# Optimization experiments

Measured on AMD Instinct MI355X. Metric: run time of the kernel, lower is better.

Reference implementation:

```python
import jax, jax.numpy as jnp
import numpy as np

T, B, N_INP, N_HID, N_OUT = 512, 128, 256, 1024, 128


def setup_inputs() -> dict:
    key = jax.random.key(0)
    ks = jax.random.split(key, 7)
    x = jax.random.normal(ks[0], (T, B, N_INP), dtype=jnp.float32)
    # PyTorch RNNCell/Linear default init: U(-1/sqrt(fan_in), 1/sqrt(fan_in))
    s_h = 1.0 / np.sqrt(N_HID)
    W_ih = jax.random.uniform(ks[1], (N_HID, N_INP), jnp.float32, -s_h, s_h)
    W_hh = jax.random.uniform(ks[2], (N_HID, N_HID), jnp.float32, -s_h, s_h)
    b_ih = jax.random.uniform(ks[3], (N_HID,), jnp.float32, -s_h, s_h)
    b_hh = jax.random.uniform(ks[4], (N_HID,), jnp.float32, -s_h, s_h)
    W_ro = jax.random.uniform(ks[5], (N_OUT, N_HID), jnp.float32, -s_h, s_h)
    b_ro = jax.random.uniform(ks[6], (N_OUT,), jnp.float32, -s_h, s_h)
    return {"x": x, "W_ih": W_ih, "W_hh": W_hh, "b_ih": b_ih,
            "b_hh": b_hh, "W_ro": W_ro, "b_ro": b_ro}


def reference(x, W_ih, W_hh, b_ih, b_hh, W_ro, b_ro):
    # x: [T, B, n_inp]; recurrence: state = tanh(x_t W_ih^T + b_ih + state W_hh^T + b_hh)
    batch = x.shape[1]
    n_hid = W_hh.shape[0]
    state0 = jnp.zeros((batch, n_hid), dtype=x.dtype)

    # Precompute the input projection for all timesteps in one big GEMM.
    x_proj = jnp.einsum('tbi,hi->tbh', x, W_ih) + b_ih + b_hh  # [T, B, n_hid]

    def step(state, xp_t):
        new_state = jnp.tanh(xp_t + state @ W_hh.T)
        return new_state, None

    final_state, _ = jax.lax.scan(step, state0, x_proj)
    # readout applied to final hidden state only (stateOnly=None path)
    return final_state @ W_ro.T + b_ro  # [B, n_out]
```

## Files before the change

kernel.cpp:

```cpp
#include <hip/hip_runtime.h>
#include <hip/hip_bf16.h>
#include <stdint.h>


#define TSTEPS 512
#define BATCH  128
#define NI     256
#define NH     1024
#define NO     128
#define NBLK   128
#define NTHR   512
#define NWAVE  8
#define BG     16
#define COLS   64

typedef __attribute__((ext_vector_type(8))) short s16x8;
typedef __attribute__((ext_vector_type(4))) float f32x4;
typedef __attribute__((ext_vector_type(4))) unsigned u32x4;
typedef unsigned long long ull;

__device__ __forceinline__ unsigned short f2bf_rne(float f) {
  unsigned u = __builtin_bit_cast(unsigned, f);
  unsigned r = u + 0x7fffu + ((u >> 16) & 1u);
  return (unsigned short)(r >> 16);
}
__device__ __forceinline__ float bf2f(unsigned short h) {
  unsigned u = ((unsigned)h) << 16;
  return __builtin_bit_cast(float, u);
}
__device__ __forceinline__ void split_bf(float v, short &hi, short &lo) {
  unsigned short h = f2bf_rne(v);
  hi = (short)h;
  lo = (short)f2bf_rne(v - bf2f(h));
}
__device__ __forceinline__ f32x4 mfma16(s16x8 a, s16x8 b, f32x4 c) {
  return __builtin_amdgcn_mfma_f32_16x16x32_bf16(a, b, c, 0, 0, 0);
}
__device__ __forceinline__ float fast_tanh(float a) {
  float cl = fminf(fmaxf(a, -15.f), 15.f);
  float e  = __expf(2.f * cl);
  return (e - 1.f) / (e + 1.f);
}

#define SIDX(g, w, r, k) ((((size_t)(g) * NWAVE + (w)) * BG + (r)) * 128 + (k))

__global__ __launch_bounds__(NTHR, 2)
void rnn_persistent(const float* __restrict__ x,
                    const float* __restrict__ W_ih,
                    const float* __restrict__ W_hh,
                    const float* __restrict__ b_ih,
                    const float* __restrict__ b_hh,
                    unsigned*    __restrict__ SP)
{
  const int tid  = threadIdx.x;
  const int wave = tid >> 6;
  const int lane = tid & 63;
  const int lr   = lane & 15;
  const int lq   = lane >> 4;
  const int g    = blockIdx.x >> 4;
  const int m    = blockIdx.x & 15;
  const int row0 = g * BG;
  const int h0   = m * COLS;
  const int kq0  = wave * 128;
  const int iq0  = wave * 32;

  __shared__ float red[2][NWAVE][1024];

  s16x8 whh_hi[4][4], whh_lo[4][4];
  #pragma unroll
  for (int nt = 0; nt < 4; ++nt) {
    const int h = h0 + nt * 16 + lr;
    #pragma unroll
    for (int kb = 0; kb < 4; ++kb) {
      const float* p = W_hh + (size_t)h * NH + kq0 + kb * 32 + lq * 8;
      s16x8 hi, lo;
      #pragma unroll
      for (int j = 0; j < 8; ++j) { short a, b; split_bf(p[j], a, b); hi[j] = a; lo[j] = b; }
      whh_hi[nt][kb] = hi; whh_lo[nt][kb] = lo;
    }
  }
  s16x8 wih_hi[4], wih_lo[4];
  #pragma unroll
  for (int nt = 0; nt < 4; ++nt) {
    const int h = h0 + nt * 16 + lr;
    const float* p = W_ih + (size_t)h * NI + iq0 + lq * 8;
    s16x8 hi, lo;
    #pragma unroll
    for (int j = 0; j < 8; ++j) { short a, b; split_bf(p[j], a, b); hi[j] = a; lo[j] = b; }
    wih_hi[nt] = hi; wih_lo[nt] = lo;
  }

  const int er = tid >> 5;
  const int ec = (tid & 31) * 2;
  const float bias0 = b_ih[h0 + ec]     + b_hh[h0 + ec];
  const float bias1 = b_ih[h0 + ec + 1] + b_hh[h0 + ec + 1];
  const int wsl = m >> 1;
  const int klo = (m & 1) * 64 + ec;

  unsigned* buf0 = SP;
  unsigned* buf1 = SP + (size_t)BATCH * NH;

  float xf[8];
  {
    const float* xp = x + (size_t)(row0 + lr) * NI + iq0 + lq * 8;
    #pragma unroll
    for (int j = 0; j < 8; ++j) xf[j] = xp[j];
  }

  const unsigned* sb0 = buf0 + SIDX(g, wave, lr, lq * 8);
  const unsigned* sb1 = buf1 + SIDX(g, wave, lr, lq * 8);

  for (int t = 0; t < TSTEPS; ++t) {
    f32x4 acc[4];
    #pragma unroll
    for (int nt = 0; nt < 4; ++nt) acc[nt] = (f32x4){0.f, 0.f, 0.f, 0.f};
    {
      s16x8 xhi, xlo;
      #pragma unroll
      for (int j = 0; j < 8; ++j) { short a, b; split_bf(xf[j], a, b); xhi[j] = a; xlo[j] = b; }
      #pragma unroll
      for (int nt = 0; nt < 4; ++nt) {
        acc[nt] = mfma16(xhi, wih_hi[nt], acc[nt]);
        acc[nt] = mfma16(xhi, wih_lo[nt], acc[nt]);
        acc[nt] = mfma16(xlo, wih_hi[nt], acc[nt]);
      }
    }
    const unsigned etag = (unsigned)((t >> 1) & 1);
    const unsigned* sb = (t & 1) ? sb1 : sb0;
    u32x4 sv0, sv1, sv2, sv3, sv4, sv5, sv6, sv7;
    {
      const u32x4 e4 = (u32x4){etag, etag, etag, etag};
      for (;;) {
        asm volatile(
          "global_load_dwordx4 %0, %8, off sc1\n\t"
          "global_load_dwordx4 %1, %8, off offset:16 sc1\n\t"
          "global_load_dwordx4 %2, %8, off offset:128 sc1\n\t"
          "global_load_dwordx4 %3, %8, off offset:144 sc1\n\t"
          "global_load_dwordx4 %4, %8, off offset:256 sc1\n\t"
          "global_load_dwordx4 %5, %8, off offset:272 sc1\n\t"
          "global_load_dwordx4 %6, %8, off offset:384 sc1\n\t"
          "global_load_dwordx4 %7, %8, off offset:400 sc1\n\t"
          "s_waitcnt vmcnt(0)"
          : "=&v"(sv0), "=&v"(sv1), "=&v"(sv2), "=&v"(sv3),
            "=&v"(sv4), "=&v"(sv5), "=&v"(sv6), "=&v"(sv7)
          : "v"(sb) : "memory");
        u32x4 b4 = (sv0 ^ e4) | (sv1 ^ e4) | (sv2 ^ e4) | (sv3 ^ e4)
                 | (sv4 ^ e4) | (sv5 ^ e4) | (sv6 ^ e4) | (sv7 ^ e4);
        unsigned bad = b4[0] | b4[1] | b4[2] | b4[3];
        if ((bad & 1u) == 0) break;
      }
    }
    {
      const int tn = (t + 1 < TSTEPS) ? (t + 1) : t;
      const float* xp = x + (size_t)tn * BATCH * NI + (size_t)(row0 + lr) * NI + iq0 + lq * 8;
      #pragma unroll
      for (int j = 0; j < 8; ++j) xf[j] = xp[j];
    }
    {
      unsigned sw[32];
      #pragma unroll
      for (int e = 0; e < 4; ++e) {
        sw[0  + e] = sv0[e]; sw[4  + e] = sv1[e];
        sw[8  + e] = sv2[e]; sw[12 + e] = sv3[e];
        sw[16 + e] = sv4[e]; sw[20 + e] = sv5[e];
        sw[24 + e] = sv6[e]; sw[28 + e] = sv7[e];
      }
      #pragma unroll
      for (int kb = 0; kb < 4; ++kb) {
        s16x8 shi, slo;
        #pragma unroll
        for (int j = 0; j < 8; ++j) {
          unsigned w = sw[kb * 8 + j];
          shi[j] = (short)(w >> 16);
          slo[j] = (short)(w & 0xffffu);
        }
        #pragma unroll
        for (int nt = 0; nt < 4; ++nt) {
          acc[nt] = mfma16(shi, whh_hi[nt][kb], acc[nt]);
          acc[nt] = mfma16(shi, whh_lo[nt][kb], acc[nt]);
          acc[nt] = mfma16(slo, whh_hi[nt][kb], acc[nt]);
        }
      }
    }
    const int rbi = t & 1;
    #pragma unroll
    for (int nt = 0; nt < 4; ++nt)
      #pragma unroll
      for (int r = 0; r < 4; ++r)
        red[rbi][wave][(lq * 4 + r) * 64 + nt * 16 + lr] = acc[nt][r];
    __syncthreads();
    {
      float s0 = bias0, s1 = bias1;
      #pragma unroll
      for (int w = 0; w < NWAVE; ++w) {
        float2 v = *(const float2*)&red[rbi][w][er * 64 + ec];
        s0 += v.x; s1 += v.y;
      }
      float t0 = fast_tanh(s0), t1 = fast_tanh(s1);
      const unsigned otag = (unsigned)(((t + 1) >> 1) & 1);
      unsigned short h0b = f2bf_rne(t0);
      unsigned       l0b = ((f2bf_rne(t0 - bf2f(h0b)) & 0xfffeu) | otag);
      unsigned short h1b = f2bf_rne(t1);
      unsigned       l1b = ((f2bf_rne(t1 - bf2f(h1b)) & 0xfffeu) | otag);
      ull pk = ((ull)(((unsigned)h1b << 16) | l1b) << 32)
             |  (ull)(((unsigned)h0b << 16) | l0b);
      ull* op = (ull*)(((t + 1) & 1 ? buf1 : buf0) + SIDX(g, wsl, er, klo));
      __hip_atomic_store(op, pk, __ATOMIC_RELAXED, __HIP_MEMORY_SCOPE_AGENT);
    }
  }
}

__global__ __launch_bounds__(256)
void init_buf1(unsigned* __restrict__ SP) {
  const int i = blockIdx.x * 256 + threadIdx.x;
  SP[BATCH * NH + i] = 1u;
}

__global__ __launch_bounds__(512)
void rnn_readout(const unsigned* __restrict__ SP,
                 const float* __restrict__ W_ro,
                 const float* __restrict__ b_ro,
                 float* __restrict__ out)
{
  __shared__ float srow[4][NH];
  const int b0 = blockIdx.x * 4;
  for (int i = threadIdx.x; i < 4 * NH; i += 512) {
    const int b = b0 + (i >> 10);
    const int h = i & 1023;
    unsigned u = SP[SIDX(b >> 4, h >> 7, b & 15, h & 127)];
    srow[i >> 10][h] = bf2f((unsigned short)(u >> 16)) + bf2f((unsigned short)(u & 0xffffu));
  }
  __syncthreads();
  const int bb = threadIdx.x >> 7;
  const int o  = threadIdx.x & 127;
  const float* wr = W_ro + (size_t)o * NH;
  float s = 0.f;
  #pragma unroll 4
  for (int k = 0; k < NH; ++k) s += srow[bb][k] * wr[k];
  out[(size_t)(b0 + bb) * NO + o] = s + b_ro[o];
}

extern "C" void kernel_launch(void* const* d_in, const int* in_sizes, int n_in,
                              void* d_out, int out_size, void* d_ws, size_t ws_size,
                              hipStream_t stream) {
  (void)in_sizes; (void)n_in; (void)out_size; (void)ws_size;
  const float* x    = (const float*)d_in[0];
  const float* W_ih = (const float*)d_in[1];
  const float* W_hh = (const float*)d_in[2];
  const float* b_ih = (const float*)d_in[3];
  const float* b_hh = (const float*)d_in[4];
  const float* W_ro = (const float*)d_in[5];
  const float* b_ro = (const float*)d_in[6];
  float* out = (float*)d_out;

  unsigned* SP = (unsigned*)d_ws;

  hipMemsetAsync(SP, 0, (size_t)BATCH * NH * sizeof(unsigned), stream);
  init_buf1<<<(BATCH * NH) / 256, 256, 0, stream>>>(SP);

  rnn_persistent<<<NBLK, NTHR, 0, stream>>>(x, W_ih, W_hh, b_ih, b_hh, SP);
  rnn_readout<<<BATCH / 4, 512, 0, stream>>>(SP, W_ro, b_ro, out);
}
```

Before: 1.944 ms.

## Drop low-order weight split and widen blocks to 128 hidden columns

Weights are now held only as a single bf16 term instead of a hi/lo split, so each state chunk needs two MFMAs per tile instead of three. The grid shrinks from 128 to 64 persistent blocks, each covering 128 hidden columns. That halves the number of blocks taking part in the per-step cross-block flag synchronisation and makes the freed register space usable for the wider tile. The shared reduction buffer becomes single-buffered and gets an extra barrier, and each thread packs and stores four outputs. Precision drops because the weights lose their low-order residual, which may raise error over 512 recurrent steps.

```diff
diff --git a/kernel.cpp b/kernel.cpp
--- a/kernel.cpp
+++ b/kernel.cpp
@@ -8,11 +8,11 @@
 #define NI     256
 #define NH     1024
 #define NO     128
-#define NBLK   128
+#define NBLK   64
 #define NTHR   512
 #define NWAVE  8
 #define BG     16
-#define COLS   64
+#define COLS   128
 
 typedef __attribute__((ext_vector_type(8))) short s16x8;
 typedef __attribute__((ext_vector_type(4))) float f32x4;
@@ -42,7 +42,7 @@
   return (e - 1.f) / (e + 1.f);
 }
 
-#define SIDX(g, w, r, k) ((((size_t)(g) * NWAVE + (w)) * BG + (r)) * 128 + (k))
+#define SIDX(g, p, r, k) ((((size_t)(g) * NWAVE + (p)) * BG + (r)) * 128 + (k))
 
 __global__ __launch_bounds__(NTHR, 2)
 void rnn_persistent(const float* __restrict__ x,
@@ -57,45 +57,44 @@
   const int lane = tid & 63;
   const int lr   = lane & 15;
   const int lq   = lane >> 4;
-  const int g    = blockIdx.x >> 4;
-  const int m    = blockIdx.x & 15;
+  const int g    = blockIdx.x & 7;
+  const int p    = blockIdx.x >> 3;
   const int row0 = g * BG;
-  const int h0   = m * COLS;
+  const int h0   = p * COLS;
   const int kq0  = wave * 128;
   const int iq0  = wave * 32;
 
-  __shared__ float red[2][NWAVE][1024];
-
-  s16x8 whh_hi[4][4], whh_lo[4][4];
+  __shared__ float red[NWAVE][BG][COLS];
+
+  s16x8 whh[8][4];
   #pragma unroll
-  for (int nt = 0; nt < 4; ++nt) {
+  for (int nt = 0; nt < 8; ++nt) {
     const int h = h0 + nt * 16 + lr;
     #pragma unroll
     for (int kb = 0; kb < 4; ++kb) {
-      const float* p = W_hh + (size_t)h * NH + kq0 + kb * 32 + lq * 8;
-      s16x8 hi, lo;
-      #pragma unroll
-      for (int j = 0; j < 8; ++j) { short a, b; split_bf(p[j], a, b); hi[j] = a; lo[j] = b; }
-      whh_hi[nt][kb] = hi; whh_lo[nt][kb] = lo;
-    }
-  }
-  s16x8 wih_hi[4], wih_lo[4];
+      const float* pw = W_hh + (size_t)h * NH + kq0 + kb * 32 + lq * 8;
+      s16x8 hi;
+      #pragma unroll
+      for (int j = 0; j < 8; ++j) hi[j] = (short)f2bf_rne(pw[j]);
+      whh[nt][kb] = hi;
+    }
+  }
+  s16x8 wih[8];
   #pragma unroll
-  for (int nt = 0; nt < 4; ++nt) {
+  for (int nt = 0; nt < 8; ++nt) {
     const int h = h0 + nt * 16 + lr;
-    const float* p = W_ih + (size_t)h * NI + iq0 + lq * 8;
-    s16x8 hi, lo;
-    #pragma unroll
-    for (int j = 0; j < 8; ++j) { short a, b; split_bf(p[j], a, b); hi[j] = a; lo[j] = b; }
-    wih_hi[nt] = hi; wih_lo[nt] = lo;
+    const float* pw = W_ih + (size_t)h * NI + iq0 + lq * 8;
+    s16x8 hi;
+    #pragma unroll
+    for (int j = 0; j < 8; ++j) hi[j] = (short)f2bf_rne(pw[j]);
+    wih[nt] = hi;
   }
 
   const int er = tid >> 5;
-  const int ec = (tid & 31) * 2;
-  const float bias0 = b_ih[h0 + ec]     + b_hh[h0 + ec];
-  const float bias1 = b_ih[h0 + ec + 1] + b_hh[h0 + ec + 1];
-  const int wsl = m >> 1;
-  const int klo = (m & 1) * 64 + ec;
+  const int ec = (tid & 31) * 4;
+  float bias[4];
+  #pragma unroll
+  for (int j = 0; j < 4; ++j) bias[j] = b_ih[h0 + ec + j] + b_hh[h0 + ec + j];
 
   unsigned* buf0 = SP;
   unsigned* buf1 = SP + (size_t)BATCH * NH;
@@ -111,18 +110,17 @@
   const unsigned* sb1 = buf1 + SIDX(g, wave, lr, lq * 8);
 
   for (int t = 0; t < TSTEPS; ++t) {
-    f32x4 acc[4];
-    #pragma unroll
-    for (int nt = 0; nt < 4; ++nt) acc[nt] = (f32x4){0.f, 0.f, 0.f, 0.f};
+    f32x4 acc[8];
+    #pragma unroll
+    for (int nt = 0; nt < 8; ++nt) acc[nt] = (f32x4){0.f, 0.f, 0.f, 0.f};
     {
       s16x8 xhi, xlo;
       #pragma unroll
       for (int j = 0; j < 8; ++j) { short a, b; split_bf(xf[j], a, b); xhi[j] = a; xlo[j] = b; }
       #pragma unroll
-      for (int nt = 0; nt < 4; ++nt) {
-        acc[nt] = mfma16(xhi, wih_hi[nt], acc[nt]);
-        acc[nt] = mfma16(xhi, wih_lo[nt], acc[nt]);
-        acc[nt] = mfma16(xlo, wih_hi[nt], acc[nt]);
+      for (int nt = 0; nt < 8; ++nt) {
+        acc[nt] = mfma16(xhi, wih[nt], acc[nt]);
+        acc[nt] = mfma16(xlo, wih[nt], acc[nt]);
       }
     }
     const unsigned etag = (unsigned)((t >> 1) & 1);
@@ -156,56 +154,51 @@
       #pragma unroll
       for (int j = 0; j < 8; ++j) xf[j] = xp[j];
     }
-    {
-      unsigned sw[32];
-      #pragma unroll
-      for (int e = 0; e < 4; ++e) {
-        sw[0  + e] = sv0[e]; sw[4  + e] = sv1[e];
-        sw[8  + e] = sv2[e]; sw[12 + e] = sv3[e];
-        sw[16 + e] = sv4[e]; sw[20 + e] = sv5[e];
-        sw[24 + e] = sv6[e]; sw[28 + e] = sv7[e];
-      }
-      #pragma unroll
-      for (int kb = 0; kb < 4; ++kb) {
-        s16x8 shi, slo;
-        #pragma unroll
-        for (int j = 0; j < 8; ++j) {
-          unsigned w = sw[kb * 8 + j];
-          shi[j] = (short)(w >> 16);
-          slo[j] = (short)(w & 0xffffu);
-        }
-        #pragma unroll
-        for (int nt = 0; nt < 4; ++nt) {
-          acc[nt] = mfma16(shi, whh_hi[nt][kb], acc[nt]);
-          acc[nt] = mfma16(shi, whh_lo[nt][kb], acc[nt]);
-          acc[nt] = mfma16(slo, whh_hi[nt][kb], acc[nt]);
-        }
-      }
-    }
-    const int rbi = t & 1;
-    #pragma unroll
-    for (int nt = 0; nt < 4; ++nt)
+    #pragma unroll
+    for (int kb = 0; kb < 4; ++kb) {
+      const u32x4 va = (kb == 0) ? sv0 : (kb == 1) ? sv2 : (kb == 2) ? sv4 : sv6;
+      const u32x4 vb = (kb == 0) ? sv1 : (kb == 1) ? sv3 : (kb == 2) ? sv5 : sv7;
+      s16x8 shi, slo;
+      #pragma unroll
+      for (int i = 0; i < 4; ++i) {
+        unsigned wa = va[i], wb = vb[i];
+        shi[i]     = (short)(wa >> 16); slo[i]     = (short)(wa & 0xffffu);
+        shi[i + 4] = (short)(wb >> 16); slo[i + 4] = (short)(wb & 0xffffu);
+      }
+      #pragma unroll
+      for (int nt = 0; nt < 8; ++nt) {
+        acc[nt] = mfma16(shi, whh[nt][kb], acc[nt]);
+        acc[nt] = mfma16(slo, whh[nt][kb], acc[nt]);
+      }
+    }
+    __syncthreads();
+    #pragma unroll
+    for (int nt = 0; nt < 8; ++nt)
       #pragma unroll
       for (int r = 0; r < 4; ++r)
-        red[rbi][wave][(lq * 4 + r) * 64 + nt * 16 + lr] = acc[nt][r];
+        red[wave][lq * 4 + r][nt * 16 + lr] = acc[nt][r];
     __syncthreads();
     {
-      float s0 = bias0, s1 = bias1;
+      float s[4] = {bias[0], bias[1], bias[2], bias[3]};
       #pragma unroll
       for (int w = 0; w < NWAVE; ++w) {
-        float2 v = *(const float2*)&red[rbi][w][er * 64 + ec];
-        s0 += v.x; s1 += v.y;
-      }
-      float t0 = fast_tanh(s0), t1 = fast_tanh(s1);
+        const f32x4 v = *(const f32x4*)&red[w][er][ec];
+        s[0] += v[0]; s[1] += v[1]; s[2] += v[2]; s[3] += v[3];
+      }
       const unsigned otag = (unsigned)(((t + 1) >> 1) & 1);
-      unsigned short h0b = f2bf_rne(t0);
-      unsigned       l0b = ((f2bf_rne(t0 - bf2f(h0b)) & 0xfffeu) | otag);
-      unsigned short h1b = f2bf_rne(t1);
-      unsigned       l1b = ((f2bf_rne(t1 - bf2f(h1b)) & 0xfffeu) | otag);
-      ull pk = ((ull)(((unsigned)h1b << 16) | l1b) << 32)
-             |  (ull)(((unsigned)h0b << 16) | l0b);
-      ull* op = (ull*)(((t + 1) & 1 ? buf1 : buf0) + SIDX(g, wsl, er, klo));
-      __hip_atomic_store(op, pk, __ATOMIC_RELAXED, __HIP_MEMORY_SCOPE_AGENT);
+      unsigned pkw[4];
+      #pragma unroll
+      for (int j = 0; j < 4; ++j) {
+        float tv = fast_tanh(s[j]);
+        unsigned short hb = f2bf_rne(tv);
+        unsigned       lb = ((f2bf_rne(tv - bf2f(hb)) & 0xfffeu) | otag);
+        pkw[j] = (((unsigned)hb) << 16) | lb;
+      }
+      ull pk01 = ((ull)pkw[1] << 32) | (ull)pkw[0];
+      ull pk23 = ((ull)pkw[3] << 32) | (ull)pkw[2];
+      ull* op = (ull*)(((t + 1) & 1 ? buf1 : buf0) + SIDX(g, p, er, ec));
+      __hip_atomic_store(op,     pk01, __ATOMIC_RELAXED, __HIP_MEMORY_SCOPE_AGENT);
+      __hip_atomic_store(op + 1, pk23, __ATOMIC_RELAXED, __HIP_MEMORY_SCOPE_AGENT);
     }
   }
 }
```

New measurement: 2.177 ms. 12.0% more time.

## Pack hi/lo bf16 pairs per dword and duplicate weights to cut MFMA count

Applied to the files above, without the earlier changes.

Replaces the three-MFMA hi/lo split-bf16 product with a packed form. Each state and input dword keeps its hi/lo bf16 halves together, and every weight is rounded once to bf16 and duplicated, so one MFMA over the K dimension forms (hi+lo)*w. This cuts recurrent MFMAs per step and removes the unpacking shuffles, but it drops the weight low-order correction, which lowers accuracy. The state loads are now issued before the input-projection MFMAs to overlap the polling latency, and the block-to-(group,column) mapping is swapped.

```diff
diff --git a/kernel.cpp b/kernel.cpp
--- a/kernel.cpp
+++ b/kernel.cpp
@@ -28,11 +28,6 @@
   unsigned u = ((unsigned)h) << 16;
   return __builtin_bit_cast(float, u);
 }
-__device__ __forceinline__ void split_bf(float v, short &hi, short &lo) {
-  unsigned short h = f2bf_rne(v);
-  hi = (short)h;
-  lo = (short)f2bf_rne(v - bf2f(h));
-}
 __device__ __forceinline__ f32x4 mfma16(s16x8 a, s16x8 b, f32x4 c) {
   return __builtin_amdgcn_mfma_f32_16x16x32_bf16(a, b, c, 0, 0, 0);
 }
@@ -41,8 +36,38 @@
   float e  = __expf(2.f * cl);
   return (e - 1.f) / (e + 1.f);
 }
+__device__ __forceinline__ unsigned packf(float v) {
+  unsigned short h = f2bf_rne(v);
+  unsigned short l = f2bf_rne(v - bf2f(h));
+  return (((unsigned)h) << 16) | (unsigned)l;
+}
 
 #define SIDX(g, w, r, k) ((((size_t)(g) * NWAVE + (w)) * BG + (r)) * 128 + (k))
+
+#define SWEEP_ISSUE(PTR)                                                   \
+  asm volatile(                                                            \
+    "global_load_dwordx4 %0, %8, off sc1\n\t"                              \
+    "global_load_dwordx4 %1, %8, off offset:64 sc1\n\t"                    \
+    "global_load_dwordx4 %2, %8, off offset:128 sc1\n\t"                   \
+    "global_load_dwordx4 %3, %8, off offset:192 sc1\n\t"                   \
+    "global_load_dwordx4 %4, %8, off offset:256 sc1\n\t"                   \
+    "global_load_dwordx4 %5, %8, off offset:320 sc1\n\t"                   \
+    "global_load_dwordx4 %6, %8, off offset:384 sc1\n\t"                   \
+    "global_load_dwordx4 %7, %8, off offset:448 sc1"                       \
+    : "=&v"(sv0), "=&v"(sv1), "=&v"(sv2), "=&v"(sv3),                      \
+      "=&v"(sv4), "=&v"(sv5), "=&v"(sv6), "=&v"(sv7)                       \
+    : "v"(PTR) : "memory")
+
+#define SWEEP_WAIT()                                                       \
+  asm volatile("s_waitcnt vmcnt(0)"                                        \
+    : "+v"(sv0), "+v"(sv1), "+v"(sv2), "+v"(sv3),                          \
+      "+v"(sv4), "+v"(sv5), "+v"(sv6), "+v"(sv7) :: "memory");             \
+  __builtin_amdgcn_sched_barrier(0)
+
+#define TAGCHECK(OUT)                                                      \
+  { u32x4 b4 = (sv0 ^ e4) | (sv1 ^ e4) | (sv2 ^ e4) | (sv3 ^ e4)           \
+             | (sv4 ^ e4) | (sv5 ^ e4) | (sv6 ^ e4) | (sv7 ^ e4);          \
+    OUT = (b4[0] | b4[1] | b4[2] | b4[3]) & 1u; }
 
 __global__ __launch_bounds__(NTHR, 2)
 void rnn_persistent(const float* __restrict__ x,
@@ -57,8 +82,8 @@
   const int lane = tid & 63;
   const int lr   = lane & 15;
   const int lq   = lane >> 4;
-  const int g    = blockIdx.x >> 4;
-  const int m    = blockIdx.x & 15;
+  const int g    = blockIdx.x & 7;
+  const int m    = blockIdx.x >> 3;
   const int row0 = g * BG;
   const int h0   = m * COLS;
   const int kq0  = wave * 128;
@@ -66,28 +91,33 @@
 
   __shared__ float red[2][NWAVE][1024];
 
-  s16x8 whh_hi[4][4], whh_lo[4][4];
+  s16x8 whhd[4][4][2];
   #pragma unroll
   for (int nt = 0; nt < 4; ++nt) {
     const int h = h0 + nt * 16 + lr;
     #pragma unroll
-    for (int kb = 0; kb < 4; ++kb) {
-      const float* p = W_hh + (size_t)h * NH + kq0 + kb * 32 + lq * 8;
-      s16x8 hi, lo;
-      #pragma unroll
-      for (int j = 0; j < 8; ++j) { short a, b; split_bf(p[j], a, b); hi[j] = a; lo[j] = b; }
-      whh_hi[nt][kb] = hi; whh_lo[nt][kb] = lo;
-    }
-  }
-  s16x8 wih_hi[4], wih_lo[4];
+    for (int kb = 0; kb < 4; ++kb)
+      #pragma unroll
+      for (int p = 0; p < 2; ++p) {
+        const float* pw = W_hh + (size_t)h * NH + kq0 + kb * 32 + p * 16 + lq * 4;
+        s16x8 f;
+        #pragma unroll
+        for (int j = 0; j < 8; ++j) f[j] = (short)f2bf_rne(pw[j >> 1]);
+        whhd[nt][kb][p] = f;
+      }
+  }
+  s16x8 wihd[4][2];
   #pragma unroll
   for (int nt = 0; nt < 4; ++nt) {
     const int h = h0 + nt * 16 + lr;
-    const float* p = W_ih + (size_t)h * NI + iq0 + lq * 8;
-    s16x8 hi, lo;
-    #pragma unroll
-    for (int j = 0; j < 8; ++j) { short a, b; split_bf(p[j], a, b); hi[j] = a; lo[j] = b; }
-    wih_hi[nt] = hi; wih_lo[nt] = lo;
+    #pragma unroll
+    for (int p = 0; p < 2; ++p) {
+      const float* pw = W_ih + (size_t)h * NI + iq0 + p * 16 + lq * 4;
+      s16x8 f;
+      #pragma unroll
+      for (int j = 0; j < 8; ++j) f[j] = (short)f2bf_rne(pw[j >> 1]);
+      wihd[nt][p] = f;
+    }
   }
 
   const int er = tid >> 5;
@@ -100,87 +130,79 @@
   unsigned* buf0 = SP;
   unsigned* buf1 = SP + (size_t)BATCH * NH;
 
-  float xf[8];
+  s16x8 xfA, xfB;
   {
-    const float* xp = x + (size_t)(row0 + lr) * NI + iq0 + lq * 8;
-    #pragma unroll
-    for (int j = 0; j < 8; ++j) xf[j] = xp[j];
-  }
-
-  const unsigned* sb0 = buf0 + SIDX(g, wave, lr, lq * 8);
-  const unsigned* sb1 = buf1 + SIDX(g, wave, lr, lq * 8);
+    const float* xp = x + (size_t)(row0 + lr) * NI + iq0 + lq * 4;
+    f32x4 v0 = *(const f32x4*)xp;
+    f32x4 v1 = *(const f32x4*)(xp + 16);
+    u32x4 a, b;
+    #pragma unroll
+    for (int d = 0; d < 4; ++d) { a[d] = packf(v0[d]); b[d] = packf(v1[d]); }
+    xfA = __builtin_bit_cast(s16x8, a);
+    xfB = __builtin_bit_cast(s16x8, b);
+  }
+
+  const unsigned* sb0 = buf0 + SIDX(g, wave, lr, lq * 4);
+  const unsigned* sb1 = buf1 + SIDX(g, wave, lr, lq * 4);
 
   for (int t = 0; t < TSTEPS; ++t) {
-    f32x4 acc[4];
-    #pragma unroll
-    for (int nt = 0; nt < 4; ++nt) acc[nt] = (f32x4){0.f, 0.f, 0.f, 0.f};
-    {
-      s16x8 xhi, xlo;
-      #pragma unroll
-      for (int j = 0; j < 8; ++j) { short a, b; split_bf(xf[j], a, b); xhi[j] = a; xlo[j] = b; }
-      #pragma unroll
-      for (int nt = 0; nt < 4; ++nt) {
-        acc[nt] = mfma16(xhi, wih_hi[nt], acc[nt]);
-        acc[nt] = mfma16(xhi, wih_lo[nt], acc[nt]);
-        acc[nt] = mfma16(xlo, wih_hi[nt], acc[nt]);
-      }
-    }
     const unsigned etag = (unsigned)((t >> 1) & 1);
     const unsigned* sb = (t & 1) ? sb1 : sb0;
     u32x4 sv0, sv1, sv2, sv3, sv4, sv5, sv6, sv7;
+    SWEEP_ISSUE(sb);
+    f32x4 acc[4];
+    #pragma unroll
+    for (int nt = 0; nt < 4; ++nt) acc[nt] = (f32x4){0.f, 0.f, 0.f, 0.f};
+    #pragma unroll
+    for (int nt = 0; nt < 4; ++nt) {
+      acc[nt] = mfma16(xfA, wihd[nt][0], acc[nt]);
+      acc[nt] = mfma16(xfB, wihd[nt][1], acc[nt]);
+    }
     {
       const u32x4 e4 = (u32x4){etag, etag, etag, etag};
-      for (;;) {
-        asm volatile(
-          "global_load_dwordx4 %0, %8, off sc1\n\t"
-          "global_load_dwordx4 %1, %8, off offset:16 sc1\n\t"
-          "global_load_dwordx4 %2, %8, off offset:128 sc1\n\t"
-          "global_load_dwordx4 %3, %8, off offset:144 sc1\n\t"
-          "global_load_dwordx4 %4, %8, off offset:256 sc1\n\t"
-          "global_load_dwordx4 %5, %8, off offset:272 sc1\n\t"
-          "global_load_dwordx4 %6, %8, off offset:384 sc1\n\t"
-          "global_load_dwordx4 %7, %8, off offset:400 sc1\n\t"
-          "s_waitcnt vmcnt(0)"
-          : "=&v"(sv0), "=&v"(sv1), "=&v"(sv2), "=&v"(sv3),
-            "=&v"(sv4), "=&v"(sv5), "=&v"(sv6), "=&v"(sv7)
-          : "v"(sb) : "memory");
-        u32x4 b4 = (sv0 ^ e4) | (sv1 ^ e4) | (sv2 ^ e4) | (sv3 ^ e4)
-                 | (sv4 ^ e4) | (sv5 ^ e4) | (sv6 ^ e4) | (sv7 ^ e4);
-        unsigned bad = b4[0] | b4[1] | b4[2] | b4[3];
-        if ((bad & 1u) == 0) break;
-      }
-    }
+      unsigned bad;
+      SWEEP_WAIT();
+      TAGCHECK(bad);
+      while (bad) {
+        SWEEP_ISSUE(sb);
+        SWEEP_WAIT();
+        TAGCHECK(bad);
+      }
+    }
+    f32x4 xv0, xv1;
     {
       const int tn = (t + 1 < TSTEPS) ? (t + 1) : t;
-      const float* xp = x + (size_t)tn * BATCH * NI + (size_t)(row0 + lr) * NI + iq0 + lq * 8;
-      #pragma unroll
-      for (int j = 0; j < 8; ++j) xf[j] = xp[j];
-    }
-    {
-      unsigned sw[32];
-      #pragma unroll
-      for (int e = 0; e < 4; ++e) {
-        sw[0  + e] = sv0[e]; sw[4  + e] = sv1[e];
-        sw[8  + e] = sv2[e]; sw[12 + e] = sv3[e];
-        sw[16 + e] = sv4[e]; sw[20 + e] = sv5[e];
-        sw[24 + e] = sv6[e]; sw[28 + e] = sv7[e];
-      }
-      #pragma unroll
-      for (int kb = 0; kb < 4; ++kb) {
-        s16x8 shi, slo;
-        #pragma unroll
-        for (int j = 0; j < 8; ++j) {
-          unsigned w = sw[kb * 8 + j];
-          shi[j] = (short)(w >> 16);
-          slo[j] = (short)(w & 0xffffu);
-        }
-        #pragma unroll
-        for (int nt = 0; nt < 4; ++nt) {
-          acc[nt] = mfma16(shi, whh_hi[nt][kb], acc[nt]);
-          acc[nt] = mfma16(shi, whh_lo[nt][kb], acc[nt]);
-          acc[nt] = mfma16(slo, whh_hi[nt][kb], acc[nt]);
-        }
-      }
+      const float* xp = x + (size_t)tn * BATCH * NI + (size_t)(row0 + lr) * NI + iq0 + lq * 4;
+      xv0 = *(const f32x4*)xp;
+      xv1 = *(const f32x4*)(xp + 16);
+    }
+    {
+      const s16x8 a0 = __builtin_bit_cast(s16x8, sv0);
+      const s16x8 a1 = __builtin_bit_cast(s16x8, sv1);
+      const s16x8 a2 = __builtin_bit_cast(s16x8, sv2);
+      const s16x8 a3 = __builtin_bit_cast(s16x8, sv3);
+      const s16x8 a4 = __builtin_bit_cast(s16x8, sv4);
+      const s16x8 a5 = __builtin_bit_cast(s16x8, sv5);
+      const s16x8 a6 = __builtin_bit_cast(s16x8, sv6);
+      const s16x8 a7 = __builtin_bit_cast(s16x8, sv7);
+      #pragma unroll
+      for (int nt = 0; nt < 4; ++nt) {
+        acc[nt] = mfma16(a0, whhd[nt][0][0], acc[nt]);
+        acc[nt] = mfma16(a1, whhd[nt][0][1], acc[nt]);
+        acc[nt] = mfma16(a2, whhd[nt][1][0], acc[nt]);
+        acc[nt] = mfma16(a3, whhd[nt][1][1], acc[nt]);
+        acc[nt] = mfma16(a4, whhd[nt][2][0], acc[nt]);
+        acc[nt] = mfma16(a5, whhd[nt][2][1], acc[nt]);
+        acc[nt] = mfma16(a6, whhd[nt][3][0], acc[nt]);
+        acc[nt] = mfma16(a7, whhd[nt][3][1], acc[nt]);
+      }
+    }
+    {
+      u32x4 a, b;
+      #pragma unroll
+      for (int d = 0; d < 4; ++d) { a[d] = packf(xv0[d]); b[d] = packf(xv1[d]); }
+      xfA = __builtin_bit_cast(s16x8, a);
+      xfB = __builtin_bit_cast(s16x8, b);
     }
     const int rbi = t & 1;
     #pragma unroll
```

New measurement: 2.371 ms. 1.22x slower.
